# Optimization experiments

Measured on AMD Instinct MI355X. Metric: run time of the kernel, lower is better.

The kernel has to match this reference:

```python
import jax, jax.numpy as jnp
import numpy as np

B, S, D = 4, 2048, 1024
H = 16
HD = D // H


def setup_inputs() -> dict:
    key = jax.random.key(0)
    ks = jax.random.split(key, 5)
    scale = 0.02
    return {
        "x": jax.random.normal(ks[0], (B, S, D), dtype=jnp.float32),
        "wq": jax.random.normal(ks[1], (D, D), dtype=jnp.float32) * scale,
        "wk": jax.random.normal(ks[2], (D, D), dtype=jnp.float32) * scale,
        "wv": jax.random.normal(ks[3], (D, D), dtype=jnp.float32) * scale,
        "wo": jax.random.normal(ks[4], (D, D), dtype=jnp.float32) * scale,
    }


def reference(x, wq, wk, wv, wo):
    b, s, _ = x.shape
    # project and split heads: [b, h, s, hd]
    def proj(w):
        return jnp.einsum('bsd,de->bse', x, w).reshape(b, s, H, HD).transpose(0, 2, 1, 3)
    q, k, v = proj(wq), proj(wk), proj(wv)
    scores = jnp.einsum('bhqd,bhkd->bhqk', q, k)
    causal = jnp.tril(jnp.ones((s, s), dtype=bool))  # True = keep
    scores = jnp.where(causal, scores, -jnp.inf)
    attn = jax.nn.softmax(scores / jnp.sqrt(jnp.float32(HD)), axis=-1)
    ctx = jnp.einsum('bhqk,bhkd->bhqd', attn, v)
    ctx = ctx.transpose(0, 2, 1, 3).reshape(b, s, D)
    return jnp.einsum('bsd,de->bse', ctx, wo)
```

## Files before the change

### kernel.cpp

```cpp
#include <hip/hip_runtime.h>

#define S_LEN 2048
#define D_DIM 1024
#define NH    16
#define HD    64
#define BATCH 4
#define M_ROWS 8192

typedef __attribute__((ext_vector_type(8))) short bf16x8;
typedef __attribute__((ext_vector_type(4))) float f32x4;
typedef __attribute__((ext_vector_type(16))) float f32x16;
typedef __attribute__((ext_vector_type(8))) unsigned short u16x8;

__device__ __forceinline__ unsigned short f2bf(float f) {
    unsigned u = __builtin_bit_cast(unsigned, f);
    u = (u + 0x7fffu + ((u >> 16) & 1u)) >> 16;
    return (unsigned short)u;
}

__device__ __forceinline__ void gload16(const void* g, void* l) {
    __builtin_amdgcn_global_load_lds((const __attribute__((address_space(1))) unsigned*)g,
                                     (__attribute__((address_space(3))) unsigned*)l,
                                     16, 0, 0);
}

template<int N> __device__ __forceinline__ void vmwait() {
    if constexpr (N == 0)      asm volatile("s_waitcnt vmcnt(0)" ::: "memory");
    else if constexpr (N == 3) asm volatile("s_waitcnt vmcnt(3)" ::: "memory");
    else if constexpr (N == 5) asm volatile("s_waitcnt vmcnt(5)" ::: "memory");
}

__device__ __forceinline__ unsigned cvtpk_bf16(float lo, float hi) {
    unsigned r;
    asm("v_cvt_pk_bf16_f32 %0, %1, %2" : "=v"(r) : "v"(lo), "v"(hi));
    return r;
}
__device__ __forceinline__ void pl32swap(unsigned &a, unsigned &b) {
    asm("v_permlane32_swap_b32 %0, %1" : "+v"(a), "+v"(b));
}

__global__ __launch_bounds__(256) void prep_k(const float* __restrict__ x,
                                              const float* __restrict__ w0, const float* __restrict__ w1,
                                              const float* __restrict__ w2, const float* __restrict__ w3,
                                              unsigned short* __restrict__ xbf,
                                              unsigned short* __restrict__ o0, unsigned short* __restrict__ o1,
                                              unsigned short* __restrict__ o2, unsigned short* __restrict__ o3) {
    __shared__ float sT[64][65];
    const int t = threadIdx.x;
    if (blockIdx.x < 4096) {
        size_t i = (size_t)blockIdx.x * 256 + t;
        const float4* xf = (const float4*)x;
        float4 a = xf[2 * i], b = xf[2 * i + 1];
        u16x8 v;
        v[0] = f2bf(a.x); v[1] = f2bf(a.y); v[2] = f2bf(a.z); v[3] = f2bf(a.w);
        v[4] = f2bf(b.x); v[5] = f2bf(b.y); v[6] = f2bf(b.z); v[7] = f2bf(b.w);
        *(u16x8*)(xbf + i * 8) = v;
        return;
    }
    const int wb = blockIdx.x - 4096;
    const int z = wb >> 8;
    const float* w; unsigned short* o;
    switch (z) {
        case 0: w = w0; o = o0; break;
        case 1: w = w1; o = o1; break;
        case 2: w = w2; o = o2; break;
        default: w = w3; o = o3; break;
    }
    const float sc = (z == 0) ? 0.18033688011112042f : 1.0f;
    const int n0 = (wb & 15) * 64, k0 = ((wb >> 4) & 15) * 64;
    const int r = t >> 4, cq = t & 15;
#pragma unroll
    for (int it = 0; it < 4; ++it) {
        int k = r + it * 16;
        float4 v = *(const float4*)&w[(size_t)(k0 + k) * D_DIM + n0 + cq * 4];
        sT[k][cq * 4 + 0] = v.x; sT[k][cq * 4 + 1] = v.y;
        sT[k][cq * 4 + 2] = v.z; sT[k][cq * 4 + 3] = v.w;
    }
    __syncthreads();
    const int n = t >> 2, ch = t & 3;
    union { unsigned short s[8]; uint4 v; } p0, p1;
#pragma unroll
    for (int j = 0; j < 8; ++j) p0.s[j] = f2bf(sT[ch * 16 + j][n] * sc);
#pragma unroll
    for (int j = 0; j < 8; ++j) p1.s[j] = f2bf(sT[ch * 16 + 8 + j][n] * sc);
    *(uint4*)&o[(size_t)(n0 + n) * D_DIM + k0 + ch * 16]     = p0.v;
    *(uint4*)&o[(size_t)(n0 + n) * D_DIM + k0 + ch * 16 + 8] = p1.v;
}

template<int MFRAG, int NFRAG, int AGLD, int BGLD>
__device__ __forceinline__ void gemm_core(const unsigned short* __restrict__ A,
                                          const unsigned short* __restrict__ Bt,
                                          unsigned short* __restrict__ sA,
                                          unsigned short* __restrict__ sB,
                                          int m0, int n0, int t,
                                          f32x4 (&acc)[MFRAG][NFRAG])
{
    constexpr int NGLD  = AGLD + BGLD;
    constexpr int ASLOT = AGLD * 4096;
    constexpr int BSLOT = BGLD * 4096;
    constexpr int NPH   = MFRAG / 2;

    const int lane = t & 63, wid = t >> 6;
    const int mm = lane & 15, quad = lane >> 4;
    const int wm = wid >> 2, wn = wid & 3;

    const int sr = t >> 2;
    const int sg = (t & 3) ^ ((sr >> 1) & 3);
    const unsigned short* asrc = A  + (size_t)(m0 + sr) * D_DIM + sg * 8;
    const unsigned short* bsrc = Bt + (size_t)(n0 + sr) * D_DIM + sg * 8;
    unsigned short* dA = sA + t * 8;
    unsigned short* dB = sB + t * 8;

    const int al = wm * (MFRAG * 16) + mm;
    const int bl = wn * (NFRAG * 16) + mm;
    const int xs = quad ^ ((mm >> 1) & 3);

#pragma unroll
    for (int pt = 0; pt < 2; ++pt) {
        const int ko = pt * 32;
#pragma unroll
        for (int i = 0; i < AGLD; ++i)
            gload16(asrc + (size_t)i * 128 * D_DIM + ko, dA + pt * ASLOT + i * 4096);
#pragma unroll
        for (int i = 0; i < BGLD; ++i)
            gload16(bsrc + (size_t)i * 128 * D_DIM + ko, dB + pt * BSLOT + i * 4096);
    }
    vmwait<NGLD>();
    __builtin_amdgcn_s_barrier();

    int sRead = 0, sWrite = 2;
    for (int T = 0; T < 32; ++T) {
        const int soA = sRead * ASLOT, soB = sRead * BSLOT;
        const int woA = sWrite * ASLOT, woB = sWrite * BSLOT;
        const int ko = (T + 2) * 32;
        const bool st = (T <= 29);

        bf16x8 bv[NFRAG];
#pragma unroll
        for (int p = 0; p < NPH; ++p) {
            if (p == 0) {
#pragma unroll
                for (int nf = 0; nf < NFRAG; ++nf)
                    bv[nf] = *(const bf16x8*)&sB[soB + (bl + nf * 16) * 32 + xs * 8];
            }
            bf16x8 af0 = *(const bf16x8*)&sA[soA + (al + (2 * p) * 16) * 32 + xs * 8];
            bf16x8 af1 = *(const bf16x8*)&sA[soA + (al + (2 * p + 1) * 16) * 32 + xs * 8];

            if (st) {
                if (p == 0) {
#pragma unroll
                    for (int i = 0; i < AGLD; ++i)
                        gload16(asrc + (size_t)i * 128 * D_DIM + ko, dA + woA + i * 4096);
                } else {
#pragma unroll
                    for (int i = 0; i < BGLD; ++i)
                        if ((i % (NPH - 1)) == p - 1)
                            gload16(bsrc + (size_t)i * 128 * D_DIM + ko, dB + woB + i * 4096);
                }
            }

            __builtin_amdgcn_s_barrier();
            asm volatile("s_waitcnt lgkmcnt(0)" ::: "memory");
            __builtin_amdgcn_s_setprio(1);
#pragma unroll
            for (int nf = 0; nf < NFRAG; ++nf) {
                acc[2 * p][nf]     = __builtin_amdgcn_mfma_f32_16x16x32_bf16(af0, bv[nf], acc[2 * p][nf], 0, 0, 0);
                acc[2 * p + 1][nf] = __builtin_amdgcn_mfma_f32_16x16x32_bf16(af1, bv[nf], acc[2 * p + 1][nf], 0, 0, 0);
            }
            __builtin_amdgcn_s_setprio(0);
            if (p == NPH - 1) {
                if (T <= 29)      vmwait<NGLD>();
                else if (T == 30) vmwait<0>();
            }
            __builtin_amdgcn_s_barrier();
        }

        sRead  = (sRead  == 2) ? 0 : sRead + 1;
        sWrite = (sWrite == 2) ? 0 : sWrite + 1;
    }
}

__global__ __launch_bounds__(512, 2) void gemmqkv_k(const unsigned short* __restrict__ A,
                                                    const unsigned short* __restrict__ Bt,
                                                    unsigned short* __restrict__ qb,
                                                    unsigned short* __restrict__ kb,
                                                    unsigned short* __restrict__ vt)
{
    __shared__ unsigned short sA[3 * 2 * 4096];
    __shared__ unsigned short sB[3 * 3 * 4096];
    const int t = threadIdx.x;
    const int bid = blockIdx.x;
    const int wg = (bid & 7) * 32 + (bid >> 3);
    const int mt = wg >> 3, nt = wg & 7;
    const int m0 = mt * 256, n0 = nt * 384;

    f32x4 acc[8][6];
#pragma unroll
    for (int i = 0; i < 8; ++i)
#pragma unroll
        for (int j = 0; j < 6; ++j) acc[i][j] = (f32x4){0.f, 0.f, 0.f, 0.f};

    gemm_core<8, 6, 2, 3>(A, Bt, sA, sB, m0, n0, t, acc);

    const int lane = t & 63, wid = t >> 6;
    const int mm = lane & 15, quad = lane >> 4;
    const int wm = wid >> 2, wn = wid & 3;

#pragma unroll
    for (int nf = 0; nf < 6; ++nf) {
        const int c0 = n0 + wn * 96 + nf * 16;
        const int widx = c0 >> 10, nl0 = c0 & 1023;
        if (widx == 2) {
            const int h = nl0 >> 6, hd = (nl0 & 63) + mm;
#pragma unroll
            for (int mf = 0; mf < 8; ++mf) {
                int rglob = m0 + wm * 128 + mf * 16 + quad * 4;
                int bb = rglob >> 11, ss = rglob & (S_LEN - 1);
                union { unsigned short s[4]; unsigned long long ll; } pk;
#pragma unroll
                for (int r = 0; r < 4; ++r) pk.s[r] = f2bf(acc[mf][nf][r]);
                *(unsigned long long*)&vt[((size_t)(bb * NH + h) * HD + hd) * S_LEN + ss] = pk.ll;
            }
        } else {
            unsigned short* outp = widx ? kb : qb;
#pragma unroll
            for (int mf = 0; mf < 8; ++mf)
#pragma unroll
                for (int r = 0; r < 4; ++r)
                    outp[(size_t)(m0 + wm * 128 + mf * 16 + quad * 4 + r) * D_DIM +
                         nl0 + mm] = f2bf(acc[mf][nf][r]);
        }
    }
}

__global__ __launch_bounds__(512, 2) void gemmo_k(const unsigned short* __restrict__ A,
                                                  const unsigned short* __restrict__ Bt,
                                                  float* __restrict__ C)
{
    __shared__ unsigned short sA[3 * 4096];
    __shared__ unsigned short sB[3 * 2 * 4096];
    const int t = threadIdx.x;
    const int bid = blockIdx.x;
    const int wg = (bid & 7) * 32 + (bid >> 3);
    const int mt = wg >> 2, nt = wg & 3;
    const int m0 = mt * 128, n0 = nt * 256;

    f32x4 acc[4][4];
#pragma unroll
    for (int i = 0; i < 4; ++i)
#pragma unroll
        for (int j = 0; j < 4; ++j) acc[i][j] = (f32x4){0.f, 0.f, 0.f, 0.f};

    gemm_core<4, 4, 1, 2>(A, Bt, sA, sB, m0, n0, t, acc);

    const int lane = t & 63, wid = t >> 6;
    const int mm = lane & 15, quad = lane >> 4;
    const int wm = wid >> 2, wn = wid & 3;

#pragma unroll
    for (int mf = 0; mf < 4; ++mf)
#pragma unroll
        for (int nf = 0; nf < 4; ++nf)
#pragma unroll
            for (int r = 0; r < 4; ++r)
                C[(size_t)(m0 + wm * 64 + mf * 16 + quad * 4 + r) * D_DIM +
                  n0 + wn * 64 + nf * 16 + mm] = acc[mf][nf][r];
}

__global__ __launch_bounds__(256, 4) void attn_k(const unsigned short* __restrict__ Q,
                                                 const unsigned short* __restrict__ K,
                                                 const unsigned short* __restrict__ Vt,
                                                 float* __restrict__ PO,
                                                 float* __restrict__ PL)
{
    __shared__ unsigned short sK [2][64 * 64];
    __shared__ unsigned short sVT[2][64 * 64];
    const int t = threadIdx.x;
    const int lane = t & 63, w = t >> 6;
    const int m5 = lane & 31, h = lane >> 5;
    const int m7 = m5 & 7;
    const int bid = blockIdx.x;
    const int xcd = bid & 7, bhl = (bid >> 3) & 7, a = bid >> 6;
    const int bh = xcd * 8 + bhl;
    const int b = bh >> 4, hh = bh & 15;
    const size_t rowbase = (size_t)b * S_LEN;
    const int coff = hh * HD;
    const unsigned short* Vh = Vt + (size_t)bh * HD * S_LEN;

    const int sc = t >> 3, sj = t & 7;
    const int sg = (sj ^ (sc & 7)) * 8;

    u16x8 onesu;
#pragma unroll
    for (int jj = 0; jj < 8; ++jj) onesu[jj] = 0x3F80;
    const bf16x8 ones = __builtin_bit_cast(bf16x8, onesu);

#pragma unroll 1
    for (int jidx = 0; jidx < 2; ++jidx) {
        const int strip = jidx ? (15 - a) : a;
        const int ktlo  = jidx ? (strip + 1) : 0;
        const int kthi  = jidx ? (2 * strip + 1) : strip;

        const int q0 = strip * 128;
        const int qrw = q0 + w * 32;
        const int qr  = qrw + m5;

        bf16x8 qf[4];
#pragma unroll
        for (int s = 0; s < 4; ++s)
            qf[s] = *(const bf16x8*)(Q + (rowbase + qr) * D_DIM + coff + s * 16 + h * 8);

        f32x16 o0, o1, l16;
#pragma unroll
        for (int r = 0; r < 16; ++r) { o0[r] = 0.f; o1[r] = 0.f; l16[r] = 0.f; }

        {
            const int k1 = ktlo * 64;
            gload16(K  + (rowbase + k1 + sc) * D_DIM + coff + sg,      (void*)&sK[0][t * 8]);
            gload16(K  + (rowbase + k1 + sc + 32) * D_DIM + coff + sg, (void*)&sK[0][2048 + t * 8]);
            gload16(Vh + (size_t)sc * S_LEN + k1 + sg,                 (void*)&sVT[0][t * 8]);
            gload16(Vh + (size_t)(sc + 32) * S_LEN + k1 + sg,          (void*)&sVT[0][2048 + t * 8]);
        }

        for (int kt = ktlo; kt <= kthi; ++kt) {
            const int buf = (kt - ktlo) & 1;
            __syncthreads();
            if (kt < kthi) {
                const int k1 = (kt + 1) * 64;
                gload16(K  + (rowbase + k1 + sc) * D_DIM + coff + sg,      (void*)&sK[1 - buf][t * 8]);
                gload16(K  + (rowbase + k1 + sc + 32) * D_DIM + coff + sg, (void*)&sK[1 - buf][2048 + t * 8]);
                gload16(Vh + (size_t)sc * S_LEN + k1 + sg,                 (void*)&sVT[1 - buf][t * 8]);
                gload16(Vh + (size_t)(sc + 32) * S_LEN + k1 + sg,          (void*)&sVT[1 - buf][2048 + t * 8]);
            }
            const int k0 = kt * 64;
            if (k0 > qrw + 31) continue;

            f32x16 s0, s1;
#pragma unroll
            for (int r = 0; r < 16; ++r) { s0[r] = 0.f; s1[r] = 0.f; }
            __builtin_amdgcn_s_setprio(1);
#pragma unroll
            for (int s = 0; s < 4; ++s) {
                const int sl = ((2 * s + h) ^ m7) * 8;
                bf16x8 ak0 = *(const bf16x8*)&sK[buf][m5 * 64 + sl];
                bf16x8 ak1 = *(const bf16x8*)&sK[buf][(32 + m5) * 64 + sl];
                s0 = __builtin_amdgcn_mfma_f32_32x32x16_bf16(ak0, qf[s], s0, 0, 0, 0);
                s1 = __builtin_amdgcn_mfma_f32_32x32x16_bf16(ak1, qf[s], s1, 0, 0, 0);
            }
            __builtin_amdgcn_s_setprio(0);

            const bool needmask = (k0 + 63) > qrw;
            bf16x8 pb[4];
#pragma unroll
            for (int kf = 0; kf < 2; ++kf) {
                unsigned pw[8];
#pragma unroll
                for (int jj = 0; jj < 8; ++jj) {
                    float plo = __builtin_amdgcn_exp2f(kf ? s1[2 * jj] : s0[2 * jj]);
                    float phi = __builtin_amdgcn_exp2f(kf ? s1[2 * jj + 1] : s0[2 * jj + 1]);
                    if (needmask) {
                        const int kb_ = k0 + kf * 32 + 4 * h;
                        const int r0 = 2 * jj, r1 = 2 * jj + 1;
                        if (kb_ + (r0 & 3) + 8 * (r0 >> 2) > qr) plo = 0.f;
                        if (kb_ + (r1 & 3) + 8 * (r1 >> 2) > qr) phi = 0.f;
                    }
                    pw[jj] = cvtpk_bf16(plo, phi);
                }
                pl32swap(pw[0], pw[2]);
                pl32swap(pw[1], pw[3]);
                pl32swap(pw[4], pw[6]);
                pl32swap(pw[5], pw[7]);
                union { unsigned u4[4]; bf16x8 v; } f0, f1;
                f0.u4[0] = pw[0]; f0.u4[1] = pw[1]; f0.u4[2] = pw[2]; f0.u4[3] = pw[3];
                f1.u4[0] = pw[4]; f1.u4[1] = pw[5]; f1.u4[2] = pw[6]; f1.u4[3] = pw[7];
                pb[kf * 2 + 0] = f0.v;
                pb[kf * 2 + 1] = f1.v;
            }

            __builtin_amdgcn_s_setprio(1);
#pragma unroll
            for (int s = 0; s < 4; ++s) {
                const int sl = ((2 * s + h) ^ m7) * 8;
                bf16x8 vf0 = *(const bf16x8*)&sVT[buf][m5 * 64 + sl];
                bf16x8 vf1 = *(const bf16x8*)&sVT[buf][(32 + m5) * 64 + sl];
                l16 = __builtin_amdgcn_mfma_f32_32x32x16_bf16(ones, pb[s], l16, 0, 0, 0);
                o0  = __builtin_amdgcn_mfma_f32_32x32x16_bf16(vf0,  pb[s], o0, 0, 0, 0);
                o1  = __builtin_amdgcn_mfma_f32_32x32x16_bf16(vf1,  pb[s], o1, 0, 0, 0);
            }
            __builtin_amdgcn_s_setprio(0);
        }
        __syncthreads();

        const int jid = ((bh << 4) + strip) * 2 + jidx;
        float* po = PO + (size_t)jid * 8192;
        const int ql = w * 32 + m5;
#pragma unroll
        for (int hf = 0; hf < 2; ++hf) {
#pragma unroll
            for (int rg = 0; rg < 4; ++rg) {
                f32x4 v;
#pragma unroll
                for (int r = 0; r < 4; ++r) v[r] = hf ? o1[rg * 4 + r] : o0[rg * 4 + r];
                *(f32x4*)&po[ql * 64 + hf * 32 + 8 * rg + 4 * h] = v;
            }
        }
        if (h == 0) PL[(size_t)jid * 128 + ql] = l16[0];
    }
}

__global__ __launch_bounds__(256) void combine_k(const float* __restrict__ PO,
                                                 const float* __restrict__ PL,
                                                 unsigned short* __restrict__ ctx)
{
    const int s = blockIdx.x;
    const int bh = s >> 4, strip = s & 15;
    const int b = bh >> 4, hh = bh & 15;
    const size_t rowbase = (size_t)b * S_LEN + strip * 128;
    const int coff = hh * HD;
    const float* p0 = PO + (size_t)s * 16384;
    const float* p1 = p0 + 8192;
    const float* l0 = PL + (size_t)s * 256;
    const float* l1 = l0 + 128;
    const int t = threadIdx.x;

#pragma unroll
    for (int k = 0; k < 8; ++k) {
        const int e = k * 1024 + t * 4;
        const int q = e >> 6, hd = e & 63;
        f32x4 va = *(const f32x4*)&p0[e];
        f32x4 vb = *(const f32x4*)&p1[e];
        const float inv = 1.f / (l0[q] + l1[q]);
        union { unsigned short s4[4]; unsigned long long ll; } pk;
#pragma unroll
        for (int r = 0; r < 4; ++r) pk.s4[r] = f2bf((va[r] + vb[r]) * inv);
        *(unsigned long long*)&ctx[(rowbase + q) * D_DIM + coff + hd] = pk.ll;
    }
}

extern "C" void kernel_launch(void* const* d_in, const int* in_sizes, int n_in,
                              void* d_out, int out_size, void* d_ws, size_t ws_size,
                              hipStream_t stream)
{
    const float* x  = (const float*)d_in[0];
    const float* wq = (const float*)d_in[1];
    const float* wk = (const float*)d_in[2];
    const float* wv = (const float*)d_in[3];
    const float* wo = (const float*)d_in[4];

    const size_t XE = (size_t)M_ROWS * D_DIM;
    const size_t WE = (size_t)D_DIM * D_DIM;
    unsigned short* ws  = (unsigned short*)d_ws;
    unsigned short* xbf = ws;
    unsigned short* wt0 = xbf + XE;
    unsigned short* wt1 = wt0 + WE;
    unsigned short* wt2 = wt1 + WE;
    unsigned short* wt3 = wt2 + WE;
    unsigned short* qb  = wt3 + WE;
    unsigned short* kb  = qb + XE;
    unsigned short* vt  = kb + XE;
    unsigned short* cb  = vt + XE;
    float* po = (float*)(cb + XE);
    float* pl = po + (size_t)2048 * 8192;

    prep_k<<<dim3(4096 + 1024), 256, 0, stream>>>(x, wq, wk, wv, wo,
                                                  xbf, wt0, wt1, wt2, wt3);

    gemmqkv_k<<<dim3(256), 512, 0, stream>>>(xbf, wt0, qb, kb, vt);

    attn_k<<<dim3(1024), 256, 0, stream>>>(qb, kb, vt, po, pl);

    combine_k<<<dim3(1024), 256, 0, stream>>>(po, pl, cb);

    gemmo_k<<<dim3(256), 512, 0, stream>>>(cb, wt3, (float*)d_out);
}
```

Before: 251.3 us.

## Retile QKV GEMM to 512x192 tiles and use nontemporal partial-output traffic

The QKV projection GEMM moves from 256x384 tiles with a 2x4 wave grid to 512x192 tiles with a 4x2 wave grid. It gets its own inline pipeline that splits each K step into two MFMA phases, with the A and B global-to-LDS loads interleaved across those phases. A new XCD-aware block mapping keeps blocks that share M rows on the same XCD. Separately, the attention partial-output stores and the combine loads become nontemporal to reduce cache pollution. The new tiling changes LDS footprint and the reuse balance between A and B, which could affect occupancy.

```diff
diff --git a/kernel.cpp b/kernel.cpp
--- a/kernel.cpp
+++ b/kernel.cpp
@@ -28,6 +28,7 @@
     if constexpr (N == 0)      asm volatile("s_waitcnt vmcnt(0)" ::: "memory");
     else if constexpr (N == 3) asm volatile("s_waitcnt vmcnt(3)" ::: "memory");
     else if constexpr (N == 5) asm volatile("s_waitcnt vmcnt(5)" ::: "memory");
+    else if constexpr (N == 6) asm volatile("s_waitcnt vmcnt(6)" ::: "memory");
 }
 
 __device__ __forceinline__ unsigned cvtpk_bf16(float lo, float hi) {
@@ -87,6 +88,130 @@
     *(uint4*)&o[(size_t)(n0 + n) * D_DIM + k0 + ch * 16 + 8] = p1.v;
 }
 
+__global__ __launch_bounds__(512, 2) void gemmqkv_k(const unsigned short* __restrict__ A,
+                                                    const unsigned short* __restrict__ Bt,
+                                                    unsigned short* __restrict__ qb,
+                                                    unsigned short* __restrict__ kb,
+                                                    unsigned short* __restrict__ vt)
+{
+    __shared__ unsigned short sA[3 * 16384];
+    __shared__ unsigned short sB[3 * 8192];
+    const int t = threadIdx.x;
+    const int lane = t & 63, wid = t >> 6;
+    const int mm = lane & 15, quad = lane >> 4;
+    const int wm = wid >> 1, wn = wid & 1;
+    const int bid = blockIdx.x;
+    const int xcd = bid & 7, ii = bid >> 3;
+    const int nt = ii & 15, mg = ii >> 4;
+    const int m0 = (xcd * 2 + mg) * 512, n0 = nt * 192;
+
+    const int sr = t >> 2;
+    const int sg = (t & 3) ^ ((sr >> 1) & 3);
+    const unsigned short* asrc = A  + (size_t)(m0 + sr) * D_DIM + sg * 8;
+    const unsigned short* bsrc = Bt + (size_t)(n0 + sr) * D_DIM + sg * 8;
+    unsigned short* dA = sA + t * 8;
+    unsigned short* dB = sB + t * 8;
+
+    const int al = wm * 128 + mm;
+    const int bl = wn * 96 + mm;
+    const int xs = quad ^ ((mm >> 1) & 3);
+
+    f32x4 acc[8][6];
+#pragma unroll
+    for (int i = 0; i < 8; ++i)
+#pragma unroll
+        for (int j = 0; j < 6; ++j) acc[i][j] = (f32x4){0.f, 0.f, 0.f, 0.f};
+
+#define STAGE_A3(SLOT_, KO_)                                                       \
+    {   _Pragma("unroll")                                                          \
+        for (int i_ = 0; i_ < 3; ++i_)                                             \
+            gload16(asrc + (size_t)i_ * 128 * D_DIM + (KO_), dA + (SLOT_) * 16384 + i_ * 4096); }
+#define STAGE_A1B2(SLOT_, KO_)                                                     \
+    {   gload16(asrc + (size_t)3 * 128 * D_DIM + (KO_), dA + (SLOT_) * 16384 + 3 * 4096); \
+        _Pragma("unroll")                                                          \
+        for (int i_ = 0; i_ < 2; ++i_)                                             \
+            gload16(bsrc + (size_t)i_ * 128 * D_DIM + (KO_), dB + (SLOT_) * 8192 + i_ * 4096); }
+
+    STAGE_A3(0, 0);  STAGE_A1B2(0, 0);
+    STAGE_A3(1, 32); STAGE_A1B2(1, 32);
+    vmwait<6>();
+    __builtin_amdgcn_s_barrier();
+
+    int sRead = 0, sWrite = 2;
+    for (int T = 0; T < 32; ++T) {
+        const int soA = sRead * 16384, soB = sRead * 8192;
+        const int ko = (T + 2) * 32;
+        const bool st = (T <= 29);
+
+        bf16x8 bv[6], af[4];
+#pragma unroll
+        for (int nf = 0; nf < 6; ++nf)
+            bv[nf] = *(const bf16x8*)&sB[soB + (bl + nf * 16) * 32 + xs * 8];
+#pragma unroll
+        for (int mf = 0; mf < 4; ++mf)
+            af[mf] = *(const bf16x8*)&sA[soA + (al + mf * 16) * 32 + xs * 8];
+        if (st) STAGE_A3(sWrite, ko);
+        __builtin_amdgcn_s_barrier();
+        asm volatile("s_waitcnt lgkmcnt(0)" ::: "memory");
+        __builtin_amdgcn_s_setprio(1);
+#pragma unroll
+        for (int mf = 0; mf < 4; ++mf)
+#pragma unroll
+            for (int nf = 0; nf < 6; ++nf)
+                acc[mf][nf] = __builtin_amdgcn_mfma_f32_16x16x32_bf16(af[mf], bv[nf], acc[mf][nf], 0, 0, 0);
+        __builtin_amdgcn_s_setprio(0);
+        __builtin_amdgcn_s_barrier();
+
+#pragma unroll
+        for (int mf = 0; mf < 4; ++mf)
+            af[mf] = *(const bf16x8*)&sA[soA + (al + (4 + mf) * 16) * 32 + xs * 8];
+        if (st) STAGE_A1B2(sWrite, ko);
+        __builtin_amdgcn_s_barrier();
+        asm volatile("s_waitcnt lgkmcnt(0)" ::: "memory");
+        __builtin_amdgcn_s_setprio(1);
+#pragma unroll
+        for (int mf = 0; mf < 4; ++mf)
+#pragma unroll
+            for (int nf = 0; nf < 6; ++nf)
+                acc[4 + mf][nf] = __builtin_amdgcn_mfma_f32_16x16x32_bf16(af[mf], bv[nf], acc[4 + mf][nf], 0, 0, 0);
+        __builtin_amdgcn_s_setprio(0);
+        if (T <= 29)      vmwait<6>();
+        else if (T == 30) vmwait<0>();
+        __builtin_amdgcn_s_barrier();
+
+        sRead  = (sRead  == 2) ? 0 : sRead + 1;
+        sWrite = (sWrite == 2) ? 0 : sWrite + 1;
+    }
+#undef STAGE_A3
+#undef STAGE_A1B2
+
+#pragma unroll
+    for (int nf = 0; nf < 6; ++nf) {
+        const int c0 = n0 + wn * 96 + nf * 16;
+        const int widx = c0 >> 10, nl0 = c0 & 1023;
+        if (widx == 2) {
+            const int h = nl0 >> 6, hd = (nl0 & 63) + mm;
+#pragma unroll
+            for (int mf = 0; mf < 8; ++mf) {
+                int rglob = m0 + wm * 128 + mf * 16 + quad * 4;
+                int bb = rglob >> 11, ss = rglob & (S_LEN - 1);
+                union { unsigned short s[4]; unsigned long long ll; } pk;
+#pragma unroll
+                for (int r = 0; r < 4; ++r) pk.s[r] = f2bf(acc[mf][nf][r]);
+                *(unsigned long long*)&vt[((size_t)(bb * NH + h) * HD + hd) * S_LEN + ss] = pk.ll;
+            }
+        } else {
+            unsigned short* outp = widx ? kb : qb;
+#pragma unroll
+            for (int mf = 0; mf < 8; ++mf)
+#pragma unroll
+                for (int r = 0; r < 4; ++r)
+                    outp[(size_t)(m0 + wm * 128 + mf * 16 + quad * 4 + r) * D_DIM +
+                         nl0 + mm] = f2bf(acc[mf][nf][r]);
+        }
+    }
+}
+
 template<int MFRAG, int NFRAG, int AGLD, int BGLD>
 __device__ __forceinline__ void gemm_core(const unsigned short* __restrict__ A,
                                           const unsigned short* __restrict__ Bt,
@@ -177,59 +302,6 @@
 
         sRead  = (sRead  == 2) ? 0 : sRead + 1;
         sWrite = (sWrite == 2) ? 0 : sWrite + 1;
-    }
-}
-
-__global__ __launch_bounds__(512, 2) void gemmqkv_k(const unsigned short* __restrict__ A,
-                                                    const unsigned short* __restrict__ Bt,
-                                                    unsigned short* __restrict__ qb,
-                                                    unsigned short* __restrict__ kb,
-                                                    unsigned short* __restrict__ vt)
-{
-    __shared__ unsigned short sA[3 * 2 * 4096];
-    __shared__ unsigned short sB[3 * 3 * 4096];
-    const int t = threadIdx.x;
-    const int bid = blockIdx.x;
-    const int wg = (bid & 7) * 32 + (bid >> 3);
-    const int mt = wg >> 3, nt = wg & 7;
-    const int m0 = mt * 256, n0 = nt * 384;
-
-    f32x4 acc[8][6];
-#pragma unroll
-    for (int i = 0; i < 8; ++i)
-#pragma unroll
-        for (int j = 0; j < 6; ++j) acc[i][j] = (f32x4){0.f, 0.f, 0.f, 0.f};
-
-    gemm_core<8, 6, 2, 3>(A, Bt, sA, sB, m0, n0, t, acc);
-
-    const int lane = t & 63, wid = t >> 6;
-    const int mm = lane & 15, quad = lane >> 4;
-    const int wm = wid >> 2, wn = wid & 3;
-
-#pragma unroll
-    for (int nf = 0; nf < 6; ++nf) {
-        const int c0 = n0 + wn * 96 + nf * 16;
-        const int widx = c0 >> 10, nl0 = c0 & 1023;
-        if (widx == 2) {
-            const int h = nl0 >> 6, hd = (nl0 & 63) + mm;
-#pragma unroll
-            for (int mf = 0; mf < 8; ++mf) {
-                int rglob = m0 + wm * 128 + mf * 16 + quad * 4;
-                int bb = rglob >> 11, ss = rglob & (S_LEN - 1);
-                union { unsigned short s[4]; unsigned long long ll; } pk;
-#pragma unroll
-                for (int r = 0; r < 4; ++r) pk.s[r] = f2bf(acc[mf][nf][r]);
-                *(unsigned long long*)&vt[((size_t)(bb * NH + h) * HD + hd) * S_LEN + ss] = pk.ll;
-            }
-        } else {
-            unsigned short* outp = widx ? kb : qb;
-#pragma unroll
-            for (int mf = 0; mf < 8; ++mf)
-#pragma unroll
-                for (int r = 0; r < 4; ++r)
-                    outp[(size_t)(m0 + wm * 128 + mf * 16 + quad * 4 + r) * D_DIM +
-                         nl0 + mm] = f2bf(acc[mf][nf][r]);
-        }
     }
 }
 
@@ -401,7 +473,7 @@
                 f32x4 v;
 #pragma unroll
                 for (int r = 0; r < 4; ++r) v[r] = hf ? o1[rg * 4 + r] : o0[rg * 4 + r];
-                *(f32x4*)&po[ql * 64 + hf * 32 + 8 * rg + 4 * h] = v;
+                __builtin_nontemporal_store(v, (f32x4*)&po[ql * 64 + hf * 32 + 8 * rg + 4 * h]);
             }
         }
         if (h == 0) PL[(size_t)jid * 128 + ql] = l16[0];
@@ -427,8 +499,8 @@
     for (int k = 0; k < 8; ++k) {
         const int e = k * 1024 + t * 4;
         const int q = e >> 6, hd = e & 63;
-        f32x4 va = *(const f32x4*)&p0[e];
-        f32x4 vb = *(const f32x4*)&p1[e];
+        f32x4 va = __builtin_nontemporal_load((const f32x4*)&p0[e]);
+        f32x4 vb = __builtin_nontemporal_load((const f32x4*)&p1[e]);
         const float inv = 1.f / (l0[q] + l1[q]);
         union { unsigned short s4[4]; unsigned long long ll; } pk;
 #pragma unroll
```

After: 248.1 us. No clear change (-1.3%).
